# Optimization experiments

Hardware: AMD Instinct MI355X
Metric: run time of the kernel (lower is better)

## Reference

```python
import jax, jax.numpy as jnp
import numpy as np


def setup_inputs() -> dict:
    key = jax.random.key(0)
    B, S, H, O, L, NH = 16, 1024, 1024, 256, 4, 8
    ks = jax.random.split(key, 10)
    s = 0.02
    return {
        "x": jax.random.normal(ks[0], (B, S, H), dtype=jnp.float32),
        "Wf": jax.random.normal(ks[1], (L, H, H), dtype=jnp.float32) * s,
        "bf": jnp.zeros((L, H), dtype=jnp.float32),
        "Wi": jax.random.normal(ks[2], (L, H, H), dtype=jnp.float32) * s,
        "bi": jnp.zeros((L, H), dtype=jnp.float32),
        "Wh": jax.random.normal(ks[3], (L, H, H), dtype=jnp.float32) * s,
        "bh": jnp.zeros((L, H), dtype=jnp.float32),
        "in_proj_w": jax.random.normal(ks[4], (3 * H, H), dtype=jnp.float32) * s,
        "in_proj_b": jnp.zeros((3 * H,), dtype=jnp.float32),
        "out_w": jax.random.normal(ks[5], (H, H), dtype=jnp.float32) * s,
        "out_b": jnp.zeros((H,), dtype=jnp.float32),
        "fc_w": jax.random.normal(ks[6], (O, H), dtype=jnp.float32) * s,
        "fc_b": jnp.zeros((O,), dtype=jnp.float32),
    }


def _min_lstm_layer(x, Wf, bf, Wi, bi, Wh, bh):
    # x: [B, S, D] -> [B, S, H]. minLSTM: h_t = f'_t * h_{t-1} + i'_t * h~_t
    f = jax.nn.sigmoid(jnp.einsum("bsd,hd->bsh", x, Wf) + bf)
    i = jax.nn.sigmoid(jnp.einsum("bsd,hd->bsh", x, Wi) + bi)
    h_tilde = jnp.einsum("bsd,hd->bsh", x, Wh) + bh
    denom = f + i
    fp = f / denom                      # decay coefficient per step
    add = (i / denom) * h_tilde         # input contribution per step
    # sequential scan over time (linear gated recurrence)
    def step(h, inp):
        fp_t, add_t = inp               # each [B, H]
        h = fp_t * h + add_t
        return h, h
    B, S, H = fp.shape
    h0 = jnp.zeros((B, H), dtype=x.dtype)
    _, hs = jax.lax.scan(step, h0, (fp.transpose(1, 0, 2), add.transpose(1, 0, 2)))
    return hs.transpose(1, 0, 2)        # [B, S, H]


def _mhsa(x, in_proj_w, in_proj_b, out_w, out_b, num_heads=8):
    B, S, H = x.shape
    dh = H // num_heads
    qkv = jnp.einsum("bsh,oh->bso", x, in_proj_w) + in_proj_b  # [B,S,3H]
    q, k, v = jnp.split(qkv, 3, axis=-1)
    def heads(t):
        return t.reshape(B, S, num_heads, dh).transpose(0, 2, 1, 3)  # [B,nh,S,dh]
    q, k, v = heads(q), heads(k), heads(v)
    scores = jnp.einsum("bnqd,bnkd->bnqk", q, k) / jnp.sqrt(jnp.float32(dh)).astype(x.dtype)
    attn = jax.nn.softmax(scores, axis=-1)
    o = jnp.einsum("bnqk,bnkd->bnqd", attn, v)
    o = o.transpose(0, 2, 1, 3).reshape(B, S, H)
    return jnp.einsum("bsh,oh->bso", o, out_w) + out_b


def reference(x, Wf, bf, Wi, bi, Wh, bh, in_proj_w, in_proj_b, out_w, out_b, fc_w, fc_b):
    out = x
    L = Wf.shape[0]
    for l in range(L):
        out = _min_lstm_layer(out, Wf[l], bf[l], Wi[l], bi[l], Wh[l], bh[l])
    attn_out = _mhsa(out, in_proj_w, in_proj_b, out_w, out_b, num_heads=8)
    out = attn_out + out                 # dropout is identity at eval
    last = out[:, -1, :]                 # [B, H]
    return jnp.einsum("bh,oh->bo", last, fc_w) + fc_b
```

## Files before the change

### kernel.cpp

```cpp
#include <hip/hip_runtime.h>
#include <hip/hip_bf16.h>
#include <math.h>

#define Bq   16
#define Sq   1024
#define Hq   1024
#define Oq   256
#define Lq   4
#define NHq  8
#define DHq  128
#define Mq   (Bq*Sq)
#define HHq  (Hq*Hq)
#define NCc  32
#define CTc  32

typedef __bf16 bf16x8 __attribute__((ext_vector_type(8)));
typedef float  f32x4  __attribute__((ext_vector_type(4)));

__device__ __forceinline__ float bf2f(unsigned int u) {
    union { unsigned int i; float f; } x; x.i = u << 16; return x.f;
}
__device__ __forceinline__ unsigned short f2bf(float f) {
    union { float f; unsigned int i; } x; x.f = f;
    unsigned int r = x.i + 0x7fffu + ((x.i >> 16) & 1u);
    return (unsigned short)(r >> 16);
}
__device__ __forceinline__ float sigm(float x) { return 1.f / (1.f + __expf(-x)); }

__device__ __forceinline__ void gl2lds16(const unsigned short* g, unsigned short* l) {
    __builtin_amdgcn_global_load_lds((const __attribute__((address_space(1))) void*)g,
                                     (__attribute__((address_space(3))) void*)l, 16, 0, 0);
}

__global__ void cvt_kernel(const float* __restrict__ src, unsigned short* __restrict__ dst, int n) {
    int i = blockIdx.x * 256 + threadIdx.x;
    if (i < n) dst[i] = f2bf(src[i]);
}

__global__ void cvtW_kernel(const float* __restrict__ Wf, const float* __restrict__ Wi,
                            const float* __restrict__ Wh, unsigned short* __restrict__ Wcat) {
    int i = blockIdx.x * 256 + threadIdx.x;
    int l = (i >> 20) / 3;
    int r = i - l * 3 * HHq;
    int g = r >> 20; int j = r & (HHq - 1);
    const float* s = (g == 0) ? Wf : (g == 1) ? Wi : Wh;
    Wcat[i] = f2bf(s[(size_t)l * HHq + j]);
}

__global__ void bias3_kernel(const float* __restrict__ bf_, const float* __restrict__ bi_,
                             const float* __restrict__ bh_, float* __restrict__ out) {
    int i = blockIdx.x * 256 + threadIdx.x;
    int l = i / (3*Hq); int r = i % (3*Hq); int g = r >> 10; int j = r & (Hq-1);
    const float* s = (g == 0) ? bf_ : (g == 1) ? bi_ : bh_;
    out[i] = s[l*Hq + j];
}

__global__ __launch_bounds__(512, 2)
void gemm_gate_kernel(const unsigned short* __restrict__ A, const unsigned short* __restrict__ Wl,
                      const float* __restrict__ bias3, unsigned short* __restrict__ FPo,
                      unsigned short* __restrict__ ADDo)
{
    const int K = Hq;
    __shared__ unsigned short lds[4 * 16384];
    const int tid  = threadIdx.x;

    const int lid = blockIdx.x;
    const int xcd = lid & 7;
    const int s   = lid >> 3;
    const int bm  = xcd * 16 + (s >> 3);
    const int cb  = s & 7;

    const int wid  = tid >> 6, lane = tid & 63;
    const int wm   = (wid >> 2) * 64;
    const int wn   = (wid & 3) * 32;
    const int l15  = lane & 15, quad = lane >> 4;

    const unsigned short* Ag = A + (size_t)(bm*128) * K;

    const int lr = lane >> 2;
    const int gc = (lane & 3) ^ ((lane >> 3) & 3);

    const int offA = (wid*16 + lr) * K + gc*8;
    const int ldsA = wid * 512;
    int offW[3], ldsW[3];
    #pragma unroll
    for (int q = 0; q < 3; ++q) {
        int rw = wid*48 + q*16 + lr;
        int g  = rw >> 7;
        int nr = rw & 127;
        offW[q] = g * HHq + (cb*128 + nr) * K + gc*8;
        ldsW[q] = 4096 + (wid*48 + q*16) * 32;
    }

    const int crd = quad ^ ((l15 >> 1) & 3);

    f32x4 acc[3][4][2] = {};

    auto STAGE = [&](int kt, int slot) {
        const int kof = kt << 5;
        unsigned short* Sb = &lds[slot * 16384];
        gl2lds16(Ag + offA + kof,    Sb + ldsA);
        gl2lds16(Wl + offW[0] + kof, Sb + ldsW[0]);
        gl2lds16(Wl + offW[1] + kof, Sb + ldsW[1]);
        gl2lds16(Wl + offW[2] + kof, Sb + ldsW[2]);
    };

    auto COMPUTE = [&](int slot) {
        const unsigned short* Sa = &lds[slot * 16384];
        const unsigned short* Sw = Sa + 4096;
        bf16x8 af[4];
        #pragma unroll
        for (int t = 0; t < 4; ++t)
            af[t] = *(const bf16x8*)&Sa[(wm + t*16 + l15)*32 + crd*8];
        bf16x8 wf[3][2];
        #pragma unroll
        for (int g = 0; g < 3; ++g)
            #pragma unroll
            for (int t = 0; t < 2; ++t)
                wf[g][t] = *(const bf16x8*)&Sw[(g*128 + wn + t*16 + l15)*32 + crd*8];
        __builtin_amdgcn_s_setprio(1);
        #pragma unroll
        for (int g = 0; g < 3; ++g)
            #pragma unroll
            for (int tm = 0; tm < 4; ++tm)
                #pragma unroll
                for (int tn = 0; tn < 2; ++tn)
                    acc[g][tm][tn] = __builtin_amdgcn_mfma_f32_16x16x32_bf16(af[tm], wf[g][tn], acc[g][tm][tn], 0, 0, 0);
        __builtin_amdgcn_s_setprio(0);
    };

    const int niter = K >> 5;

    STAGE(0, 0);
    STAGE(1, 1);

    for (int t = 0; t < niter - 2; ++t) {
        STAGE(t + 2, (t + 2) & 3);
        asm volatile("s_waitcnt vmcnt(8) lgkmcnt(0)" ::: "memory");
        __builtin_amdgcn_s_barrier();
        asm volatile("" ::: "memory");
        COMPUTE(t & 3);
    }
    asm volatile("s_waitcnt vmcnt(4) lgkmcnt(0)" ::: "memory");
    __builtin_amdgcn_s_barrier();
    asm volatile("" ::: "memory");
    COMPUTE((niter - 2) & 3);
    asm volatile("s_waitcnt vmcnt(0) lgkmcnt(0)" ::: "memory");
    __builtin_amdgcn_s_barrier();
    asm volatile("" ::: "memory");
    COMPUTE((niter - 1) & 3);

    #pragma unroll
    for (int tm = 0; tm < 4; ++tm) {
        int row0 = bm*128 + wm + tm*16 + quad*4;
        #pragma unroll
        for (int tn = 0; tn < 2; ++tn) {
            int col = cb*128 + wn + tn*16 + l15;
            float bf_ = bias3[col], bi_ = bias3[Hq + col], bh_ = bias3[2*Hq + col];
            #pragma unroll
            for (int r = 0; r < 4; ++r) {
                float f  = sigm(acc[0][tm][tn][r] + bf_);
                float i  = sigm(acc[1][tm][tn][r] + bi_);
                float ht = acc[2][tm][tn][r] + bh_;
                float rd = 1.f / (f + i);
                size_t off = (size_t)(row0 + r) * Hq + col;
                FPo[off]  = f2bf(f * rd);
                ADDo[off] = f2bf(i * rd * ht);
            }
        }
    }
}

__global__ __launch_bounds__(256)
void gemm_bt_kernel(const unsigned short* __restrict__ A, const unsigned short* __restrict__ W,
                    const float* __restrict__ bias, unsigned short* __restrict__ C,
                    int N, int K, int nbn)
{
    __shared__ unsigned short As[2*4096];
    __shared__ unsigned short Ws[2*4096];
    const int tid  = threadIdx.x;

    const int lid = blockIdx.x;
    const int xcd = lid & 7;
    const int s   = lid >> 3;
    const int bm  = xcd * 16 + s / nbn;
    const int bn  = s % nbn;

    const int wid  = tid >> 6, lane = tid & 63;
    const int wm   = (wid >> 1) * 64, wn = (wid & 1) * 64;
    const int l15  = lane & 15, quad = lane >> 4;

    const unsigned short* Ag = A + (size_t)(bm*128) * K;
    const unsigned short* Wg = W + (size_t)(bn*128) * K;

    const int r0   = wid*32 + (lane >> 2);
    const int cst  = (lane & 3) ^ ((r0 >> 1) & 3);
    const size_t g0 = (size_t)r0 * K + cst*8;
    const size_t g1 = (size_t)(r0 + 16) * K + cst*8;
    const int lofs0 = wid*1024;
    const int lofs1 = wid*1024 + 512;

    const int crd = quad ^ ((l15 >> 1) & 3);

    f32x4 acc[4][4] = {};

    const int niter = K >> 5;

    gl2lds16(Ag + g0, &As[lofs0]);
    gl2lds16(Ag + g1, &As[lofs1]);
    gl2lds16(Wg + g0, &Ws[lofs0]);
    gl2lds16(Wg + g1, &Ws[lofs1]);
    __syncthreads();

    for (int it = 0; it < niter; ++it) {
        const int cur = it & 1;
        if (it + 1 < niter) {
            const int nxt = (it + 1) & 1;
            const size_t k1 = (size_t)(it + 1) << 5;
            gl2lds16(Ag + g0 + k1, &As[nxt*4096 + lofs0]);
            gl2lds16(Ag + g1 + k1, &As[nxt*4096 + lofs1]);
            gl2lds16(Wg + g0 + k1, &Ws[nxt*4096 + lofs0]);
            gl2lds16(Wg + g1 + k1, &Ws[nxt*4096 + lofs1]);
        }
        bf16x8 af[4], wf[4];
        #pragma unroll
        for (int t = 0; t < 4; ++t) {
            af[t] = *(const bf16x8*)&As[cur*4096 + (wm + t*16 + l15)*32 + crd*8];
            wf[t] = *(const bf16x8*)&Ws[cur*4096 + (wn + t*16 + l15)*32 + crd*8];
        }
        #pragma unroll
        for (int tm = 0; tm < 4; ++tm)
            #pragma unroll
            for (int tn = 0; tn < 4; ++tn)
                acc[tm][tn] = __builtin_amdgcn_mfma_f32_16x16x32_bf16(af[tm], wf[tn], acc[tm][tn], 0, 0, 0);
        __syncthreads();
    }

    #pragma unroll
    for (int tm = 0; tm < 4; ++tm) {
        int row0 = bm*128 + wm + tm*16 + quad*4;
        #pragma unroll
        for (int tn = 0; tn < 4; ++tn) {
            int col = bn*128 + wn + tn*16 + l15;
            float bv = bias[col];
            #pragma unroll
            for (int r = 0; r < 4; ++r)
                C[(size_t)(row0 + r) * N + col] = f2bf(acc[tm][tn][r] + bv);
        }
    }
}

__global__ __launch_bounds__(256)
void scan_sum_kernel(const unsigned short* __restrict__ FP, const unsigned short* __restrict__ AD,
                     float* __restrict__ Ps, float* __restrict__ Asum) {
    int bid = blockIdx.x;
    int tid = threadIdx.x;
    int b = bid >> 6; int r = bid & 63; int chunk = r >> 1; int jb = r & 1;
    int j = jb*512 + tid*2;
    size_t base = ((size_t)(b*Sq + chunk*CTc)) * Hq + j;
    float P0 = 1.f, P1 = 1.f, A0 = 0.f, A1 = 0.f;
    for (int s = 0; s < CTc; ++s) {
        size_t ro = base + (size_t)s * Hq;
        unsigned int uf = *(const unsigned int*)(FP + ro);
        unsigned int ua = *(const unsigned int*)(AD + ro);
        float fp0 = bf2f(uf & 0xffffu), fp1 = bf2f(uf >> 16);
        float ad0 = bf2f(ua & 0xffffu), ad1 = bf2f(ua >> 16);
        P0 *= fp0; A0 = fp0 * A0 + ad0;
        P1 *= fp1; A1 = fp1 * A1 + ad1;
    }
    int oi = (b*NCc + chunk)*Hq + j;
    Ps[oi] = P0; Ps[oi+1] = P1;
    Asum[oi] = A0; Asum[oi+1] = A1;
}

__global__ void scan_base_kernel(const float* __restrict__ Ps, const float* __restrict__ Asum,
                                 float* __restrict__ Hb) {
    int t = blockIdx.x * 256 + threadIdx.x;
    int b = t >> 10, j = t & 1023;
    float h = 0.f;
    for (int c = 0; c < NCc; ++c) {
        int idx = (b*NCc + c)*Hq + j;
        Hb[idx] = h;
        h = Ps[idx] * h + Asum[idx];
    }
}

__global__ __launch_bounds__(256)
void scan_out_kernel(const unsigned short* __restrict__ FP, const unsigned short* __restrict__ AD,
                     const float* __restrict__ Hb, unsigned short* __restrict__ Ho) {
    int bid = blockIdx.x;
    int tid = threadIdx.x;
    int b = bid >> 6; int r = bid & 63; int chunk = r >> 1; int jb = r & 1;
    int j = jb*512 + tid*2;
    size_t base = ((size_t)(b*Sq + chunk*CTc)) * Hq + j;
    int oi = (b*NCc + chunk)*Hq + j;
    float h0 = Hb[oi], h1 = Hb[oi+1];
    for (int s = 0; s < CTc; ++s) {
        size_t ro = base + (size_t)s * Hq;
        unsigned int uf = *(const unsigned int*)(FP + ro);
        unsigned int ua = *(const unsigned int*)(AD + ro);
        h0 = bf2f(uf & 0xffffu) * h0 + bf2f(ua & 0xffffu);
        h1 = bf2f(uf >> 16)     * h1 + bf2f(ua >> 16);
        unsigned int packed = (unsigned int)f2bf(h0) | ((unsigned int)f2bf(h1) << 16);
        *(unsigned int*)(Ho + ro) = packed;
    }
}

__global__ void xlast_kernel(const unsigned short* __restrict__ act, float* __restrict__ xl) {
    int i = blockIdx.x * 256 + threadIdx.x;
    int b = i >> 10, j = i & 1023;
    xl[i] = bf2f((unsigned int)act[((size_t)(b*Sq + Sq-1)) * Hq + j]);
}

__global__ __launch_bounds__(256)
void gemv_kernel(const float* __restrict__ W, const float* __restrict__ xv,
                 const float* __restrict__ bias, const float* __restrict__ resid,
                 float* __restrict__ out, int N) {
    int b = blockIdx.x;
    int w = threadIdx.x >> 6, lane = threadIdx.x & 63;
    int n = blockIdx.y*4 + w;
    __shared__ float xs[Hq];
    *(float4*)&xs[threadIdx.x*4] = *(const float4*)&xv[(size_t)b*Hq + threadIdx.x*4];
    __syncthreads();
    const float4* wr = (const float4*)(W + (size_t)n * Hq);
    float a = 0.f;
    #pragma unroll
    for (int c = 0; c < 4; ++c) {
        float4 wv = wr[c*64 + lane];
        float4 x4 = *(const float4*)&xs[c*256 + lane*4];
        a += wv.x*x4.x + wv.y*x4.y + wv.z*x4.z + wv.w*x4.w;
    }
    #pragma unroll
    for (int st = 32; st > 0; st >>= 1) a += __shfl_xor(a, st, 64);
    if (lane == 0) out[(size_t)b*N + n] = a + bias[n] + (resid ? resid[(size_t)b*Hq + n] : 0.f);
}

__global__ __launch_bounds__(1024)
void attn_kernel(const unsigned short* __restrict__ KV,
                 const float* __restrict__ q, float* __restrict__ o) {
    int b = blockIdx.x >> 3, nh = blockIdx.x & 7;
    int tid = threadIdx.x;
    __shared__ float qs[DHq];
    __shared__ float p[Sq];
    __shared__ float redw[16];
    __shared__ float red2[16*DHq];
    if (tid < DHq) qs[tid] = q[b*Hq + nh*DHq + tid] * 0.08838834764831845f;
    __syncthreads();

    const int g = tid >> 4, l = tid & 15;
    const unsigned short* Kb = KV + (size_t)b*Sq*2048 + nh*DHq;
    float lmax = -1e30f;
    #pragma unroll 4
    for (int it = 0; it < 16; ++it) {
        int s = it*64 + g;
        union { uint4 v; unsigned short u[8]; } kk;
        kk.v = *(const uint4*)(Kb + (size_t)s*2048 + l*8);
        float a = 0.f;
        #pragma unroll
        for (int j = 0; j < 8; ++j) a += bf2f((unsigned int)kk.u[j]) * qs[l*8 + j];
        a += __shfl_xor(a, 1, 16);
        a += __shfl_xor(a, 2, 16);
        a += __shfl_xor(a, 4, 16);
        a += __shfl_xor(a, 8, 16);
        if (l == 0) p[s] = a;
        lmax = fmaxf(lmax, a);
    }
    #pragma unroll
    for (int st = 32; st > 0; st >>= 1) lmax = fmaxf(lmax, __shfl_xor(lmax, st, 64));
    if ((tid & 63) == 0) redw[tid >> 6] = lmax;
    __syncthreads();
    float mx = redw[0];
    #pragma unroll
    for (int i = 1; i < 16; ++i) mx = fmaxf(mx, redw[i]);

    float e = __expf(p[tid] - mx);
    float ls = e;
    #pragma unroll
    for (int st = 32; st > 0; st >>= 1) ls += __shfl_xor(ls, st, 64);
    __syncthreads();
    p[tid] = e;
    if ((tid & 63) == 0) redw[tid >> 6] = ls;
    __syncthreads();
    float ssum = 0.f;
    #pragma unroll
    for (int i = 0; i < 16; ++i) ssum += redw[i];
    float inv = 1.f / ssum;

    int d2 = (tid & 63) * 2, sb = tid >> 6;
    const unsigned short* Vb = KV + (size_t)b*Sq*2048 + 1024 + nh*DHq + d2;
    float a0 = 0.f, a1 = 0.f;
    for (int s = sb*64; s < sb*64 + 64; ++s) {
        unsigned int vv = *(const unsigned int*)(Vb + (size_t)s*2048);
        float pw = p[s];
        a0 += pw * bf2f(vv & 0xffffu);
        a1 += pw * bf2f(vv >> 16);
    }
    red2[sb*DHq + d2] = a0;
    red2[sb*DHq + d2 + 1] = a1;
    __syncthreads();
    if (tid < DHq) {
        float a = 0.f;
        #pragma unroll
        for (int i = 0; i < 16; ++i) a += red2[i*DHq + tid];
        o[b*Hq + nh*DHq + tid] = a * inv;
    }
}

extern "C" void kernel_launch(void* const* d_in, const int* in_sizes, int n_in,
                              void* d_out, int out_size, void* d_ws, size_t ws_size,
                              hipStream_t stream) {
    const float* x        = (const float*)d_in[0];
    const float* Wf       = (const float*)d_in[1];
    const float* bfv      = (const float*)d_in[2];
    const float* Wi       = (const float*)d_in[3];
    const float* biv      = (const float*)d_in[4];
    const float* Wh       = (const float*)d_in[5];
    const float* bhv      = (const float*)d_in[6];
    const float* in_proj_w= (const float*)d_in[7];
    const float* in_proj_b= (const float*)d_in[8];
    const float* out_w    = (const float*)d_in[9];
    const float* out_b    = (const float*)d_in[10];
    const float* fc_w     = (const float*)d_in[11];
    const float* fc_b     = (const float*)d_in[12];
    float* outp = (float*)d_out;

    char* p = (char*)d_ws;
    auto alloc = [&](size_t bytes) -> void* {
        void* r = (void*)p; p += (bytes + 255) & ~(size_t)255; return r;
    };
    unsigned short* Wcat = (unsigned short*)alloc((size_t)Lq*3*HHq*2);
    unsigned short* Wkv  = (unsigned short*)alloc((size_t)2048*Hq*2);
    float*          Bias3= (float*)alloc((size_t)Lq*3*Hq*4);
    unsigned short* actA = (unsigned short*)alloc((size_t)Mq*Hq*2);
    unsigned short* actB = (unsigned short*)alloc((size_t)Mq*Hq*2);
    unsigned short* FPg  = (unsigned short*)alloc((size_t)Mq*Hq*2);
    unsigned short* ADDg = (unsigned short*)alloc((size_t)Mq*Hq*2);
    float* Ps   = (float*)alloc((size_t)Bq*NCc*Hq*4);
    float* Asum = (float*)alloc((size_t)Bq*NCc*Hq*4);
    float* Hb   = (float*)alloc((size_t)Bq*NCc*Hq*4);
    unsigned short* KV = FPg;
    float* xl   = (float*)alloc((size_t)Bq*Hq*4);
    float* qbuf = (float*)alloc((size_t)Bq*Hq*4);
    float* obuf = (float*)alloc((size_t)Bq*Hq*4);
    float* rbuf = (float*)alloc((size_t)Bq*Hq*4);

    cvt_kernel<<<Mq*Hq/256, 256, 0, stream>>>(x, actA, Mq*Hq);
    cvtW_kernel<<<Lq*3*HHq/256, 256, 0, stream>>>(Wf, Wi, Wh, Wcat);
    cvt_kernel<<<2048*Hq/256, 256, 0, stream>>>(in_proj_w + (size_t)Hq*Hq, Wkv, 2048*Hq);
    bias3_kernel<<<(Lq*3*Hq)/256, 256, 0, stream>>>(bfv, biv, bhv, Bias3);

    unsigned short* cur = actA;
    unsigned short* nxt = actB;
    for (int l = 0; l < Lq; ++l) {
        gemm_gate_kernel<<<(Mq/128)*(Hq/128), 512, 0, stream>>>(
            cur, Wcat + (size_t)l*3*HHq, Bias3 + l*3*Hq, FPg, ADDg);
        scan_sum_kernel<<<Bq*NCc*2, 256, 0, stream>>>(FPg, ADDg, Ps, Asum);
        scan_base_kernel<<<Bq*Hq/256, 256, 0, stream>>>(Ps, Asum, Hb);
        scan_out_kernel<<<Bq*NCc*2, 256, 0, stream>>>(FPg, ADDg, Hb, nxt);
        unsigned short* t = cur; cur = nxt; nxt = t;
    }

    gemm_bt_kernel<<<(Mq/128)*(2048/128), 256, 0, stream>>>(
        cur, Wkv, in_proj_b + Hq, KV, 2048, Hq, 2048/128);
    xlast_kernel<<<Bq*Hq/256, 256, 0, stream>>>(cur, xl);
    gemv_kernel<<<dim3(Bq, Hq/4), 256, 0, stream>>>(in_proj_w, xl, in_proj_b, nullptr, qbuf, Hq);
    attn_kernel<<<Bq*NHq, 1024, 0, stream>>>(KV, qbuf, obuf);
    gemv_kernel<<<dim3(Bq, Hq/4), 256, 0, stream>>>(out_w, obuf, out_b, xl, rbuf, Hq);
    gemv_kernel<<<dim3(Bq, Oq/4), 256, 0, stream>>>(fc_w, rbuf, fc_b, nullptr, outp, Oq);
}
```

Before: 876.5 us.

## Shrink gate GEMM tile to 128x64 and add 4-stage pipeline to KV GEMM

The gate GEMM block tile drops from 128 rows x 128 columns per gate (512 threads) to 128 x 64 per gate (256 threads). That doubles the grid, cuts LDS use, and means each warp now stages two A chunks per k-step. The KV projection GEMM moves from a double-buffered loop with __syncthreads to the same 4-slot staged pipeline with vmcnt waits, s_setprio around the MFMAs, and a request for two blocks per CU. The aim is better occupancy and memory/compute overlap. The cost is lower data reuse per tile in the gate GEMM and more LDS per block in the KV GEMM.

```diff
diff --git a/kernel.cpp b/kernel.cpp
--- a/kernel.cpp
+++ b/kernel.cpp
@@ -55,40 +55,44 @@
     out[i] = s[l*Hq + j];
 }
 
-__global__ __launch_bounds__(512, 2)
+__global__ __launch_bounds__(256, 2)
 void gemm_gate_kernel(const unsigned short* __restrict__ A, const unsigned short* __restrict__ Wl,
                       const float* __restrict__ bias3, unsigned short* __restrict__ FPo,
                       unsigned short* __restrict__ ADDo)
 {
     const int K = Hq;
-    __shared__ unsigned short lds[4 * 16384];
+    __shared__ unsigned short lds[4 * 10240];
     const int tid  = threadIdx.x;
 
     const int lid = blockIdx.x;
     const int xcd = lid & 7;
     const int s   = lid >> 3;
-    const int bm  = xcd * 16 + (s >> 3);
-    const int cb  = s & 7;
+    const int bm  = xcd * 16 + (s >> 4);
+    const int cb  = s & 15;
 
     const int wid  = tid >> 6, lane = tid & 63;
-    const int wm   = (wid >> 2) * 64;
-    const int wn   = (wid & 3) * 32;
+    const int wm   = (wid >> 1) * 64;
+    const int wn   = (wid & 1) * 32;
     const int l15  = lane & 15, quad = lane >> 4;
 
     const unsigned short* Ag = A + (size_t)(bm*128) * K;
 
-    const int lr = lane >> 2;
-    const int gc = (lane & 3) ^ ((lane >> 3) & 3);
-
-    const int offA = (wid*16 + lr) * K + gc*8;
-    const int ldsA = wid * 512;
+    const int lr   = lane >> 2;
+    const int gc   = (lane & 3) ^ ((lane >> 3) & 3);
+    int offA[2], ldsA[2];
+    #pragma unroll
+    for (int q = 0; q < 2; ++q) {
+        int ra = wid*32 + q*16 + lr;
+        offA[q] = ra * K + gc*8;
+        ldsA[q] = (wid*32 + q*16) * 32;
+    }
     int offW[3], ldsW[3];
     #pragma unroll
     for (int q = 0; q < 3; ++q) {
         int rw = wid*48 + q*16 + lr;
-        int g  = rw >> 7;
-        int nr = rw & 127;
-        offW[q] = g * HHq + (cb*128 + nr) * K + gc*8;
+        int g  = rw >> 6;
+        int nr = rw & 63;
+        offW[q] = g * HHq + (cb*64 + nr) * K + gc*8;
         ldsW[q] = 4096 + (wid*48 + q*16) * 32;
     }
 
@@ -98,15 +102,15 @@
 
     auto STAGE = [&](int kt, int slot) {
         const int kof = kt << 5;
-        unsigned short* Sb = &lds[slot * 16384];
-        gl2lds16(Ag + offA + kof,    Sb + ldsA);
-        gl2lds16(Wl + offW[0] + kof, Sb + ldsW[0]);
-        gl2lds16(Wl + offW[1] + kof, Sb + ldsW[1]);
-        gl2lds16(Wl + offW[2] + kof, Sb + ldsW[2]);
+        unsigned short* Sb = &lds[slot * 10240];
+        #pragma unroll
+        for (int q = 0; q < 2; ++q) gl2lds16(Ag + offA[q] + kof, Sb + ldsA[q]);
+        #pragma unroll
+        for (int q = 0; q < 3; ++q) gl2lds16(Wl + offW[q] + kof, Sb + ldsW[q]);
     };
 
     auto COMPUTE = [&](int slot) {
-        const unsigned short* Sa = &lds[slot * 16384];
+        const unsigned short* Sa = &lds[slot * 10240];
         const unsigned short* Sw = Sa + 4096;
         bf16x8 af[4];
         #pragma unroll
@@ -117,7 +121,7 @@
         for (int g = 0; g < 3; ++g)
             #pragma unroll
             for (int t = 0; t < 2; ++t)
-                wf[g][t] = *(const bf16x8*)&Sw[(g*128 + wn + t*16 + l15)*32 + crd*8];
+                wf[g][t] = *(const bf16x8*)&Sw[(g*64 + wn + t*16 + l15)*32 + crd*8];
         __builtin_amdgcn_s_setprio(1);
         #pragma unroll
         for (int g = 0; g < 3; ++g)
@@ -136,12 +140,12 @@
 
     for (int t = 0; t < niter - 2; ++t) {
         STAGE(t + 2, (t + 2) & 3);
-        asm volatile("s_waitcnt vmcnt(8) lgkmcnt(0)" ::: "memory");
+        asm volatile("s_waitcnt vmcnt(10) lgkmcnt(0)" ::: "memory");
         __builtin_amdgcn_s_barrier();
         asm volatile("" ::: "memory");
         COMPUTE(t & 3);
     }
-    asm volatile("s_waitcnt vmcnt(4) lgkmcnt(0)" ::: "memory");
+    asm volatile("s_waitcnt vmcnt(5) lgkmcnt(0)" ::: "memory");
     __builtin_amdgcn_s_barrier();
     asm volatile("" ::: "memory");
     COMPUTE((niter - 2) & 3);
@@ -155,7 +159,7 @@
         int row0 = bm*128 + wm + tm*16 + quad*4;
         #pragma unroll
         for (int tn = 0; tn < 2; ++tn) {
-            int col = cb*128 + wn + tn*16 + l15;
+            int col = cb*64 + wn + tn*16 + l15;
             float bf_ = bias3[col], bi_ = bias3[Hq + col], bh_ = bias3[2*Hq + col];
             #pragma unroll
             for (int r = 0; r < 4; ++r) {
@@ -171,13 +175,12 @@
     }
 }
 
-__global__ __launch_bounds__(256)
+__global__ __launch_bounds__(256, 2)
 void gemm_bt_kernel(const unsigned short* __restrict__ A, const unsigned short* __restrict__ W,
                     const float* __restrict__ bias, unsigned short* __restrict__ C,
                     int N, int K, int nbn)
 {
-    __shared__ unsigned short As[2*4096];
-    __shared__ unsigned short Ws[2*4096];
+    __shared__ unsigned short lds[4 * 8192];
     const int tid  = threadIdx.x;
 
     const int lid = blockIdx.x;
@@ -195,8 +198,8 @@
 
     const int r0   = wid*32 + (lane >> 2);
     const int cst  = (lane & 3) ^ ((r0 >> 1) & 3);
-    const size_t g0 = (size_t)r0 * K + cst*8;
-    const size_t g1 = (size_t)(r0 + 16) * K + cst*8;
+    const int g0   = r0 * K + cst*8;
+    const int g1   = (r0 + 16) * K + cst*8;
     const int lofs0 = wid*1024;
     const int lofs1 = wid*1024 + 512;
 
@@ -204,37 +207,53 @@
 
     f32x4 acc[4][4] = {};
 
-    const int niter = K >> 5;
-
-    gl2lds16(Ag + g0, &As[lofs0]);
-    gl2lds16(Ag + g1, &As[lofs1]);
-    gl2lds16(Wg + g0, &Ws[lofs0]);
-    gl2lds16(Wg + g1, &Ws[lofs1]);
-    __syncthreads();
-
-    for (int it = 0; it < niter; ++it) {
-        const int cur = it & 1;
-        if (it + 1 < niter) {
-            const int nxt = (it + 1) & 1;
-            const size_t k1 = (size_t)(it + 1) << 5;
-            gl2lds16(Ag + g0 + k1, &As[nxt*4096 + lofs0]);
-            gl2lds16(Ag + g1 + k1, &As[nxt*4096 + lofs1]);
-            gl2lds16(Wg + g0 + k1, &Ws[nxt*4096 + lofs0]);
-            gl2lds16(Wg + g1 + k1, &Ws[nxt*4096 + lofs1]);
+    auto STAGE = [&](int kt, int slot) {
+        const int kof = kt << 5;
+        unsigned short* Sb = &lds[slot * 8192];
+        gl2lds16(Ag + g0 + kof, Sb + lofs0);
+        gl2lds16(Ag + g1 + kof, Sb + lofs1);
+        gl2lds16(Wg + g0 + kof, Sb + 4096 + lofs0);
+        gl2lds16(Wg + g1 + kof, Sb + 4096 + lofs1);
+    };
+
+    auto COMPUTE = [&](int slot) {
+        const unsigned short* Sa = &lds[slot * 8192];
+        const unsigned short* Sw = Sa + 4096;
+        bf16x8 af[4], wf[4];
+        #pragma unroll
+        for (int t = 0; t < 4; ++t) {
+            af[t] = *(const bf16x8*)&Sa[(wm + t*16 + l15)*32 + crd*8];
+            wf[t] = *(const bf16x8*)&Sw[(wn + t*16 + l15)*32 + crd*8];
         }
-        bf16x8 af[4], wf[4];
-        #pragma unroll
-        for (int t = 0; t < 4; ++t) {
-            af[t] = *(const bf16x8*)&As[cur*4096 + (wm + t*16 + l15)*32 + crd*8];
-            wf[t] = *(const bf16x8*)&Ws[cur*4096 + (wn + t*16 + l15)*32 + crd*8];
-        }
+        __builtin_amdgcn_s_setprio(1);
         #pragma unroll
         for (int tm = 0; tm < 4; ++tm)
             #pragma unroll
             for (int tn = 0; tn < 4; ++tn)
                 acc[tm][tn] = __builtin_amdgcn_mfma_f32_16x16x32_bf16(af[tm], wf[tn], acc[tm][tn], 0, 0, 0);
-        __syncthreads();
-    }
+        __builtin_amdgcn_s_setprio(0);
+    };
+
+    const int niter = K >> 5;
+
+    STAGE(0, 0);
+    STAGE(1, 1);
+
+    for (int it = 0; it < niter - 2; ++it) {
+        STAGE(it + 2, (it + 2) & 3);
+        asm volatile("s_waitcnt vmcnt(8) lgkmcnt(0)" ::: "memory");
+        __builtin_amdgcn_s_barrier();
+        asm volatile("" ::: "memory");
+        COMPUTE(it & 3);
+    }
+    asm volatile("s_waitcnt vmcnt(4) lgkmcnt(0)" ::: "memory");
+    __builtin_amdgcn_s_barrier();
+    asm volatile("" ::: "memory");
+    COMPUTE((niter - 2) & 3);
+    asm volatile("s_waitcnt vmcnt(0) lgkmcnt(0)" ::: "memory");
+    __builtin_amdgcn_s_barrier();
+    asm volatile("" ::: "memory");
+    COMPUTE((niter - 1) & 3);
 
     #pragma unroll
     for (int tm = 0; tm < 4; ++tm) {
@@ -452,7 +471,7 @@
     unsigned short* cur = actA;
     unsigned short* nxt = actB;
     for (int l = 0; l < Lq; ++l) {
-        gemm_gate_kernel<<<(Mq/128)*(Hq/128), 512, 0, stream>>>(
+        gemm_gate_kernel<<<(Mq/128)*16, 256, 0, stream>>>(
             cur, Wcat + (size_t)l*3*HHq, Bias3 + l*3*Hq, FPg, ADDg);
         scan_sum_kernel<<<Bq*NCc*2, 256, 0, stream>>>(FPg, ADDg, Ps, Asum);
         scan_base_kernel<<<Bq*Hq/256, 256, 0, stream>>>(Ps, Asum, Hb);
```

Measured after the change: 891.4 us. About the same (+1.7%).
